# Kernel tuning notes

Measured on AMD Instinct MI355X. Metric: run time of the kernel, lower is better.

## Reference

```python
import jax, jax.numpy as jnp
import numpy as np


def setup_inputs() -> dict:
    key = jax.random.key(0)
    ks = jax.random.split(key, 16)
    B, S, D = 2, 2048, 1024
    H, SH, RH = 16, 1, 3
    hd = D // H
    w = 1.0 / np.sqrt(D)
    return {
        "x": jax.random.normal(ks[0], (B, S, D), jnp.float32),
        "Wq": jax.random.normal(ks[1], (D, D), jnp.float32) * w,
        "bq": jnp.zeros((D,), jnp.float32),
        "Wk": jax.random.normal(ks[2], (D, D), jnp.float32) * w,
        "bk": jnp.zeros((D,), jnp.float32),
        "Wv": jax.random.normal(ks[3], (D, D), jnp.float32) * w,
        "bv": jnp.zeros((D,), jnp.float32),
        "Wproj": jax.random.normal(ks[4], (D, D), jnp.float32) * w,
        "bproj": jnp.zeros((D,), jnp.float32),
        "Wr": jax.random.normal(ks[5], (D, H - SH), jnp.float32) * w,
        "br": jnp.zeros((H - SH,), jnp.float32),
        "Ws": jax.random.normal(ks[6], (D, 2), jnp.float32) * w,
        "bs": jnp.zeros((2,), jnp.float32),
        "temperature": jnp.zeros((H, 1, 1), jnp.float32),
        "query_embedding": jax.random.truncated_normal(ks[7], -2.0, 2.0, (H, 1, hd), jnp.float32) * 0.02,
        "num_heads": H,
        "shared_heads": SH,
        "routed_heads": RH,
    }


def reference(x, Wq, bq, Wk, bk, Wv, bv, Wproj, bproj, Wr, br, Ws, bs,
              temperature, query_embedding, num_heads, shared_heads, routed_heads):
    B, S, D = x.shape
    H = num_heads
    hd = D // H

    def split_heads(t):  # [B,S,D] -> [B,H,S,hd]
        return t.reshape(B, S, H, hd).transpose(0, 2, 1, 3)

    q = split_heads(x @ Wq + bq)
    k = split_heads(x @ Wk + bk)
    v = split_heads(x @ Wv + bv)

    # L2-normalize q along head_dim, add learned query embedding, scale by softplus(temperature)
    q_norm = q * jax.lax.rsqrt(jnp.sum(q * q, axis=-1, keepdims=True) + 1e-12)
    q_scaled = (q_norm + query_embedding[None]) * jax.nn.softplus(temperature)[None]

    attn = jnp.einsum('bhqd,bhkd->bhqk', q_scaled, k) / jnp.sqrt(jnp.float32(hd))
    attn = jax.nn.softmax(attn, axis=-1)
    o = jnp.einsum('bhqk,bhkd->bhqd', attn, v)
    o = o.transpose(0, 2, 1, 3).reshape(B, S, D)  # [B,S,D]

    # Routed-head gating via top-k router
    gates = jax.nn.softmax(o @ Wr + br, axis=-1)          # [B,S,H-SH]
    _, idx = jax.lax.top_k(gates, routed_heads)           # [B,S,RH]
    mask = jax.nn.one_hot(idx, H - shared_heads, dtype=gates.dtype).sum(axis=2)
    routed_gates = gates * mask * jnp.float32(routed_heads)

    # Shared-head gating
    sw = jax.nn.softmax(o @ Ws + bs, axis=-1)             # [B,S,2]
    shared_gates = sw * jnp.float32(shared_heads)
    w0 = sw * 2.0
    shared_gates = w0[..., 0:1] * shared_gates
    routed_gates = w0[..., 1:2] * routed_gates
    masked_gates = jnp.concatenate([shared_gates, routed_gates], axis=-1)

    # einsum('bnh,bnd->bnd') sums over h: scales o by sum of gates
    o = masked_gates.sum(axis=-1, keepdims=True) * o
    return o @ Wproj + bproj
```

## Files before the change

### kernel.cpp

```cpp
#include <hip/hip_runtime.h>
#include <hip/hip_bf16.h>

typedef unsigned short ushort_t;
typedef unsigned int uint_t;

typedef __attribute__((ext_vector_type(8))) short bf8;
typedef __attribute__((ext_vector_type(4))) float f4;
typedef __attribute__((ext_vector_type(16))) float f16v;

__device__ __forceinline__ float bf2f(ushort_t u) {
    unsigned int x = ((unsigned int)u) << 16;
    return __uint_as_float(x);
}
__device__ __forceinline__ ushort_t f2bf(float f) {
    unsigned int x = __float_as_uint(f);
    unsigned int r = x + 0x7fffu + ((x >> 16) & 1u);
    return (ushort_t)(r >> 16);
}
__device__ __forceinline__ uint_t pack2bf(float a, float b) {
    return (uint_t)f2bf(a) | ((uint_t)f2bf(b) << 16);
}
__device__ __forceinline__ uint_t pack2bf_fast(float a, float b) {
    uint_t au = __float_as_uint(a) + 0x8000u;
    uint_t bu = __float_as_uint(b) + 0x8000u;
    return __builtin_amdgcn_perm(bu, au, 0x07060302);
}

__device__ __forceinline__ void gl2lds16(const ushort_t* g, ushort_t* l) {
    __builtin_amdgcn_global_load_lds(
        (const __attribute__((address_space(1))) void*)g,
        (__attribute__((address_space(3))) void*)l, 16, 0, 0);
}

__global__ __launch_bounds__(256)
void prep(const float* __restrict__ x, ushort_t* __restrict__ xb,
          const float* __restrict__ Wr, const float* __restrict__ Ws,
          ushort_t* __restrict__ Wg,
          const float* __restrict__ W0, const float* __restrict__ W1,
          const float* __restrict__ W2, const float* __restrict__ W3,
          ushort_t* __restrict__ T0, ushort_t* __restrict__ T1,
          ushort_t* __restrict__ T2, ushort_t* __restrict__ T3)
{
    __shared__ float tile[32][33];
    int bid = blockIdx.x;
    int t = threadIdx.x;
    if (bid < 4096) {
        int i = bid * 256 + t;
        float4 v = ((const float4*)x)[i];
        uint2 o;
        o.x = pack2bf(v.x, v.y);
        o.y = pack2bf(v.z, v.w);
        ((uint2*)xb)[i] = o;
    } else if (bid < 4224) {
        int idx = (bid - 4096) * 256 + t;
        int c = idx >> 10, d = idx & 1023;
        float v = 0.f;
        if (c < 15) v = Wr[(size_t)d * 15 + c];
        else if (c < 17) v = Ws[(size_t)d * 2 + (c - 15)];
        Wg[idx] = f2bf(v);
    } else {
        int idx = bid - 4224;
        int z = idx >> 10, r10 = idx & 1023;
        int k0 = (r10 & 31) * 32, n0 = (r10 >> 5) * 32;
        const float* W; ushort_t* T;
        switch (z) {
            case 0: W = W0; T = T0; break;
            case 1: W = W1; T = T1; break;
            case 2: W = W2; T = T2; break;
            default: W = W3; T = T3; break;
        }
        int r = t >> 3, c4 = (t & 7) * 4;
        float4 v = *(const float4*)&W[(size_t)(k0 + r) * 1024 + n0 + c4];
        tile[r][c4 + 0] = v.x; tile[r][c4 + 1] = v.y;
        tile[r][c4 + 2] = v.z; tile[r][c4 + 3] = v.w;
        __syncthreads();
        int n = t >> 3, kk = (t & 7) * 4;
        uint2 o;
        o.x = pack2bf(tile[kk][n], tile[kk + 1][n]);
        o.y = pack2bf(tile[kk + 2][n], tile[kk + 3][n]);
        *(uint2*)&T[(size_t)(n0 + n) * 1024 + k0 + kk] = o;
    }
}

__global__ __launch_bounds__(256)
void gemmQKV(const ushort_t* __restrict__ A, const ushort_t* __restrict__ Wt3,
             const float* __restrict__ bq, const float* __restrict__ bk,
             const float* __restrict__ bv,
             ushort_t* __restrict__ Qb, ushort_t* __restrict__ Kw,
             ushort_t* __restrict__ VTw,
             const float* __restrict__ temp, const float* __restrict__ emb)
{
    const int K = 1024;
    __shared__ ushort_t As[128 * 32];
    __shared__ ushort_t Bs[128 * 32];

    int t = threadIdx.x;
    int m0 = blockIdx.x * 128;
    int y = blockIdx.y;
    int region = y >> 3;
    int n0 = (y & 7) * 128;

    int lane = t & 63, w = t >> 6;
    int lm = lane & 15, quad = lane >> 4;
    int wm = (w >> 1) * 64, wn = (w & 1) * 64;

    f4 acc[4][4] = {};

    const ushort_t* pA = &A[(size_t)(m0 + (t >> 2)) * K + (t & 3) * 8];
    const ushort_t* pB = &Wt3[(size_t)(y * 128 + (t >> 2)) * K + (t & 3) * 8];
    ushort_t* lA = &As[t * 8];
    ushort_t* lB = &Bs[t * 8];
    const size_t rstep = (size_t)64 * K;

    for (int k0 = 0; k0 < K; k0 += 32) {
        gl2lds16(pA, lA);
        gl2lds16(pA + rstep, lA + 2048);
        gl2lds16(pB, lB);
        gl2lds16(pB + rstep, lB + 2048);
        pA += 32; pB += 32;
        __syncthreads();

        bf8 af[4], bfr[4];
        #pragma unroll
        for (int mi = 0; mi < 4; mi++)
            af[mi] = *(bf8*)&As[(wm + mi * 16 + lm) * 32 + quad * 8];
        #pragma unroll
        for (int ni = 0; ni < 4; ni++)
            bfr[ni] = *(bf8*)&Bs[(wn + ni * 16 + lm) * 32 + quad * 8];
        if (region == 2) {
            #pragma unroll
            for (int mi = 0; mi < 4; mi++)
            #pragma unroll
            for (int ni = 0; ni < 4; ni++)
                acc[mi][ni] = __builtin_amdgcn_mfma_f32_16x16x32_bf16(af[mi], bfr[ni], acc[mi][ni], 0, 0, 0);
        } else {
            #pragma unroll
            for (int ni = 0; ni < 4; ni++)
            #pragma unroll
            for (int mi = 0; mi < 4; mi++)
                acc[ni][mi] = __builtin_amdgcn_mfma_f32_16x16x32_bf16(bfr[ni], af[mi], acc[ni][mi], 0, 0, 0);
        }
        __syncthreads();
    }

    if (region == 0) {
        int head = (n0 + wn) >> 6;
        float sp = log1pf(__expf(temp[head]));
        f4 bv4[4], ev4[4];
        #pragma unroll
        for (int ni = 0; ni < 4; ni++) {
            bv4[ni] = *(const f4*)&bq[n0 + wn + ni * 16 + quad * 4];
            ev4[ni] = *(const f4*)&emb[head * 64 + ni * 16 + quad * 4];
        }
        #pragma unroll
        for (int mi = 0; mi < 4; mi++) {
            float v[4][4];
            float ss = 0.f;
            #pragma unroll
            for (int ni = 0; ni < 4; ni++)
            #pragma unroll
            for (int i = 0; i < 4; i++) {
                v[ni][i] = acc[ni][mi][i] + bv4[ni][i];
                ss += v[ni][i] * v[ni][i];
            }
            ss += __shfl_xor(ss, 16, 64);
            ss += __shfl_xor(ss, 32, 64);
            float rs = rsqrtf(ss + 1e-12f);
            int tok = m0 + wm + mi * 16 + lm;
            int b = tok >> 11, s = tok & 2047;
            size_t rowb = (((size_t)(b * 16 + head)) * 2048 + s) * 64;
            #pragma unroll
            for (int ni = 0; ni < 4; ni++) {
                uint2 o;
                o.x = pack2bf((v[ni][0] * rs + ev4[ni][0]) * sp * 0.125f,
                              (v[ni][1] * rs + ev4[ni][1]) * sp * 0.125f);
                o.y = pack2bf((v[ni][2] * rs + ev4[ni][2]) * sp * 0.125f,
                              (v[ni][3] * rs + ev4[ni][3]) * sp * 0.125f);
                *(uint2*)&Qb[rowb + ni * 16 + quad * 4] = o;
            }
        }
    } else if (region == 1) {
        int head = (n0 + wn) >> 6;
        f4 bv4[4];
        #pragma unroll
        for (int ni = 0; ni < 4; ni++)
            bv4[ni] = *(const f4*)&bk[n0 + wn + ni * 16 + quad * 4];
        #pragma unroll
        for (int mi = 0; mi < 4; mi++) {
            int tok = m0 + wm + mi * 16 + lm;
            int b = tok >> 11, s = tok & 2047;
            size_t rowb = (((size_t)(b * 16 + head)) * 2048 + s) * 64;
            #pragma unroll
            for (int ni = 0; ni < 4; ni++) {
                uint2 o;
                o.x = pack2bf(acc[ni][mi][0] + bv4[ni][0], acc[ni][mi][1] + bv4[ni][1]);
                o.y = pack2bf(acc[ni][mi][2] + bv4[ni][2], acc[ni][mi][3] + bv4[ni][3]);
                *(uint2*)&Kw[rowb + ni * 16 + quad * 4] = o;
            }
        }
    } else {
        float bvv[4];
        #pragma unroll
        for (int ni = 0; ni < 4; ni++) bvv[ni] = bv[n0 + wn + ni * 16 + lm];
        #pragma unroll
        for (int mi = 0; mi < 4; mi++) {
            int gr0 = m0 + wm + mi * 16 + quad * 4;
            int b = gr0 >> 11, s0 = gr0 & 2047;
            #pragma unroll
            for (int ni = 0; ni < 4; ni++) {
                int gc = n0 + wn + ni * 16 + lm;
                int h = gc >> 6, d = gc & 63;
                uint2 o;
                o.x = pack2bf(acc[mi][ni][0] + bvv[ni], acc[mi][ni][1] + bvv[ni]);
                o.y = pack2bf(acc[mi][ni][2] + bvv[ni], acc[mi][ni][3] + bvv[ni]);
                *(uint2*)&VTw[(((size_t)(b * 16 + h)) * 64 + d) * 2048 + s0] = o;
            }
        }
    }
}

__global__ __launch_bounds__(256)
void gemmP(const ushort_t* __restrict__ A, const ushort_t* __restrict__ Wt,
           const float* __restrict__ bias, const float* __restrict__ G,
           float* __restrict__ out, int M, int N, int K)
{
    __shared__ ushort_t As[128 * 32];
    __shared__ ushort_t Bs[128 * 32];

    int t = threadIdx.x;
    int m0 = blockIdx.x * 128, n0 = blockIdx.y * 128;
    int lane = t & 63, w = t >> 6;
    int lm = lane & 15, quad = lane >> 4;
    int wm = (w >> 1) * 64, wn = (w & 1) * 64;

    f4 acc[4][4] = {};

    const ushort_t* pA = &A[(size_t)(m0 + (t >> 2)) * K + (t & 3) * 8];
    const ushort_t* pB = &Wt[(size_t)(n0 + (t >> 2)) * K + (t & 3) * 8];
    ushort_t* lA = &As[t * 8];
    ushort_t* lB = &Bs[t * 8];
    const size_t rstep = (size_t)64 * K;

    for (int k0 = 0; k0 < K; k0 += 32) {
        gl2lds16(pA, lA);
        gl2lds16(pA + rstep, lA + 2048);
        gl2lds16(pB, lB);
        gl2lds16(pB + rstep, lB + 2048);
        pA += 32; pB += 32;
        __syncthreads();

        bf8 af[4], bfr[4];
        #pragma unroll
        for (int mi = 0; mi < 4; mi++)
            af[mi] = *(bf8*)&As[(wm + mi * 16 + lm) * 32 + quad * 8];
        #pragma unroll
        for (int ni = 0; ni < 4; ni++)
            bfr[ni] = *(bf8*)&Bs[(wn + ni * 16 + lm) * 32 + quad * 8];
        #pragma unroll
        for (int ni = 0; ni < 4; ni++)
        #pragma unroll
        for (int mi = 0; mi < 4; mi++)
            acc[ni][mi] = __builtin_amdgcn_mfma_f32_16x16x32_bf16(bfr[ni], af[mi], acc[ni][mi], 0, 0, 0);
        __syncthreads();
    }

    f4 bv4[4];
    #pragma unroll
    for (int ni = 0; ni < 4; ni++)
        bv4[ni] = *(const f4*)&bias[n0 + wn + ni * 16 + quad * 4];
    #pragma unroll
    for (int mi = 0; mi < 4; mi++) {
        int tok = m0 + wm + mi * 16 + lm;
        float g = G[tok];
        size_t rowb = (size_t)tok * N + n0 + wn;
        #pragma unroll
        for (int ni = 0; ni < 4; ni++) {
            f4 o;
            #pragma unroll
            for (int i = 0; i < 4; i++) o[i] = g * acc[ni][mi][i] + bv4[ni][i];
            *(f4*)&out[rowb + ni * 16 + quad * 4] = o;
        }
    }
}

__global__ __launch_bounds__(256)
void attn(const ushort_t* __restrict__ Q, const ushort_t* __restrict__ K,
          const ushort_t* __restrict__ VT, ushort_t* __restrict__ Opart,
          float* __restrict__ Lw)
{
    __shared__ ushort_t Ks[64 * 72];
    __shared__ ushort_t Vt[64 * 72];

    int t = threadIdx.x, lane = t & 63, w = t >> 6;
    int l31 = lane & 31;
    uint_t hi = lane >> 5;
    int bid = blockIdx.x;
    int bh = bid & 31, qt = (bid >> 5) & 15, ks = bid >> 9;
    size_t base = (size_t)bh * 2048 * 64;

    int tok = qt * 128 + w * 32 + l31;
    const ushort_t* qp = &Q[base + (size_t)tok * 64 + hi * 8];
    bf8 qa[4];
    #pragma unroll
    for (int c = 0; c < 4; c++) qa[c] = *(const bf8*)(qp + c * 16);

    float l_part = 0.f;
    f16v o_acc[2] = {};

    int sr = t >> 3, sc = (t & 7) * 8;
    const ushort_t* kg0 = &K[base + (size_t)sr * 64 + sc];
    const ushort_t* vg0 = &VT[base + (size_t)sr * 2048 + sc];

    int kend = ks * 1024 + 1024;
    for (int kb = ks * 1024; kb < kend; kb += 64) {
        __syncthreads();
        {
            uint4 k0 = *(const uint4*)(kg0 + (size_t)kb * 64);
            uint4 k1 = *(const uint4*)(kg0 + (size_t)(kb + 32) * 64);
            uint4 v0 = *(const uint4*)(vg0 + kb);
            uint4 v1 = *(const uint4*)(vg0 + 32 * 2048 + kb);
            *(uint4*)&Ks[sr * 72 + sc] = k0;
            *(uint4*)&Ks[(sr + 32) * 72 + sc] = k1;
            *(uint4*)&Vt[sr * 72 + sc] = v0;
            *(uint4*)&Vt[(sr + 32) * 72 + sc] = v1;
        }
        __syncthreads();

        bf8 pf[4];
        #pragma unroll
        for (int kt2 = 0; kt2 < 2; kt2++) {
            f16v s = {};
            #pragma unroll
            for (int c = 0; c < 4; c++) {
                bf8 kf = *(bf8*)&Ks[(kt2 * 32 + l31) * 72 + c * 16 + hi * 8];
                s = __builtin_amdgcn_mfma_f32_32x32x16_bf16(kf, qa[c], s, 0, 0, 0);
            }
            uint2 pk[4];
            #pragma unroll
            for (int g = 0; g < 4; g++) {
                float p0 = __expf(s[g * 4 + 0]);
                float p1 = __expf(s[g * 4 + 1]);
                float p2 = __expf(s[g * 4 + 2]);
                float p3 = __expf(s[g * 4 + 3]);
                l_part += (p0 + p1) + (p2 + p3);
                pk[g].x = pack2bf_fast(p0, p1);
                pk[g].y = pack2bf_fast(p2, p3);
            }
            #pragma unroll
            for (int cc = 0; cc < 2; cc++) {
                uint_t sx = hi ? pk[2 * cc].x : pk[2 * cc + 1].x;
                uint_t sy = hi ? pk[2 * cc].y : pk[2 * cc + 1].y;
                uint_t rx = (uint_t)__shfl_xor((int)sx, 32, 64);
                uint_t ry = (uint_t)__shfl_xor((int)sy, 32, 64);
                uint4 u;
                u.x = hi ? rx : pk[2 * cc].x;
                u.y = hi ? ry : pk[2 * cc].y;
                u.z = hi ? pk[2 * cc + 1].x : rx;
                u.w = hi ? pk[2 * cc + 1].y : ry;
                pf[kt2 * 2 + cc] = *(bf8*)&u;
            }
        }

        #pragma unroll
        for (int c = 0; c < 4; c++) {
            #pragma unroll
            for (int dt = 0; dt < 2; dt++) {
                bf8 vf = *(bf8*)&Vt[(dt * 32 + l31) * 72 + c * 16 + hi * 8];
                o_acc[dt] = __builtin_amdgcn_mfma_f32_32x32x16_bf16(vf, pf[c], o_acc[dt], 0, 0, 0);
            }
        }
    }

    l_part += __shfl_xor(l_part, 32, 64);
    if (hi == 0) Lw[((size_t)ks * 32 + bh) * 2048 + tok] = l_part;

    size_t pbase = (((size_t)(ks * 32 + bh)) * 2048 + tok) * 64;
    #pragma unroll
    for (int dt = 0; dt < 2; dt++)
    #pragma unroll
    for (int g = 0; g < 4; g++) {
        int d0 = dt * 32 + g * 8 + hi * 4;
        uint2 o;
        o.x = pack2bf_fast(o_acc[dt][g * 4 + 0], o_acc[dt][g * 4 + 1]);
        o.y = pack2bf_fast(o_acc[dt][g * 4 + 2], o_acc[dt][g * 4 + 3]);
        *(uint2*)&Opart[pbase + d0] = o;
    }
}

__global__ __launch_bounds__(256)
void combine(const ushort_t* __restrict__ Opart, const float* __restrict__ Lw,
             ushort_t* __restrict__ Ob)
{
    int i = blockIdx.x * 256 + threadIdx.x;
    int flat = i * 4;
    int row = flat >> 6;
    int d = flat & 63;
    int bh = row >> 11, tok = row & 2047;
    int b = bh >> 4, h = bh & 15;
    float rl = 1.f / (Lw[row] + Lw[65536 + row]);
    uint2 p0 = *(const uint2*)&Opart[flat];
    uint2 p1 = *(const uint2*)&Opart[4194304 + flat];
    float v0 = (bf2f(p0.x & 0xffff) + bf2f(p1.x & 0xffff)) * rl;
    float v1 = (bf2f(p0.x >> 16)   + bf2f(p1.x >> 16))   * rl;
    float v2 = (bf2f(p0.y & 0xffff) + bf2f(p1.y & 0xffff)) * rl;
    float v3 = (bf2f(p0.y >> 16)   + bf2f(p1.y >> 16))   * rl;
    uint2 o;
    o.x = pack2bf(v0, v1);
    o.y = pack2bf(v2, v3);
    *(uint2*)&Ob[((size_t)(b * 2048 + tok)) * 1024 + h * 64 + d] = o;
}

__global__ __launch_bounds__(256)
void router(const ushort_t* __restrict__ O, const ushort_t* __restrict__ Wg,
            const float* __restrict__ br, const float* __restrict__ bs,
            float* __restrict__ G)
{
    __shared__ float Ls[64][21];
    int t = threadIdx.x, lane = t & 63, w = t >> 6;
    int lm = lane & 15, quad = lane >> 4;
    int tok0 = blockIdx.x * 64;

    const ushort_t* ap = &O[(size_t)(tok0 + w * 16 + lm) * 1024 + quad * 8];
    const ushort_t* b0p = &Wg[(size_t)lm * 1024 + quad * 8];
    const ushort_t* b1p = &Wg[(size_t)(16 + lm) * 1024 + quad * 8];

    f4 acc0 = {}, acc1 = {};
    for (int k0 = 0; k0 < 1024; k0 += 32) {
        bf8 a = *(const bf8*)(ap + k0);
        bf8 b0 = *(const bf8*)(b0p + k0);
        bf8 b1 = *(const bf8*)(b1p + k0);
        acc0 = __builtin_amdgcn_mfma_f32_16x16x32_bf16(a, b0, acc0, 0, 0, 0);
        acc1 = __builtin_amdgcn_mfma_f32_16x16x32_bf16(a, b1, acc1, 0, 0, 0);
    }
    #pragma unroll
    for (int i = 0; i < 4; i++) {
        int tl = w * 16 + quad * 4 + i;
        Ls[tl][lm] = acc0[i];
        if (lm == 0) Ls[tl][16] = acc1[i];
    }
    __syncthreads();
    if (t < 64) {
        float v[15];
        float mx = -1e30f;
        #pragma unroll
        for (int c = 0; c < 15; c++) { v[c] = Ls[t][c] + br[c]; mx = fmaxf(mx, v[c]); }
        float sum = 0.f;
        #pragma unroll
        for (int c = 0; c < 15; c++) { v[c] = __expf(v[c] - mx); sum += v[c]; }
        float inv = 1.f / sum;
        float t3 = 0.f;
        for (int r = 0; r < 3; r++) {
            int bi = 0; float bv = -1e30f;
            #pragma unroll
            for (int c = 0; c < 15; c++) if (v[c] > bv) { bv = v[c]; bi = c; }
            t3 += bv; v[bi] = -1e30f;
        }
        t3 *= inv;
        float a0 = Ls[t][15] + bs[0], a1 = Ls[t][16] + bs[1];
        float m2 = fmaxf(a0, a1);
        float e0 = __expf(a0 - m2), e1 = __expf(a1 - m2);
        G[tok0 + t] = (2.f * e0 + 6.f * e1 * t3) / (e0 + e1);
    }
}

extern "C" void kernel_launch(void* const* d_in, const int* in_sizes, int n_in,
                              void* d_out, int out_size, void* d_ws, size_t ws_size,
                              hipStream_t stream)
{
    const float* x     = (const float*)d_in[0];
    const float* Wq    = (const float*)d_in[1];
    const float* bq    = (const float*)d_in[2];
    const float* Wk    = (const float*)d_in[3];
    const float* bk    = (const float*)d_in[4];
    const float* Wv    = (const float*)d_in[5];
    const float* bv    = (const float*)d_in[6];
    const float* Wproj = (const float*)d_in[7];
    const float* bproj = (const float*)d_in[8];
    const float* Wr    = (const float*)d_in[9];
    const float* br    = (const float*)d_in[10];
    const float* Ws    = (const float*)d_in[11];
    const float* bs    = (const float*)d_in[12];
    const float* temp  = (const float*)d_in[13];
    const float* emb   = (const float*)d_in[14];

    const int M = 4096, N = 1024, Kd = 1024;

    char* ws = (char*)d_ws;
    ushort_t* Kw    = (ushort_t*)ws;
    ushort_t* VTw   = (ushort_t*)(ws + 8388608);
    ushort_t* Qb    = (ushort_t*)(ws + 16777216);
    ushort_t* Wtp   = (ushort_t*)(ws + 25165824);
    float*    Gw    = (float*)(ws + 27262976);
    ushort_t* Wg    = (ushort_t*)(ws + 27279360);
    float*    Lw    = (float*)(ws + 27344896);
    ushort_t* Wt3   = (ushort_t*)(ws + 27869184);
    ushort_t* xb    = (ushort_t*)(ws + 34160640);
    ushort_t* Opart = (ushort_t*)(ws + 27869184);
    ushort_t* Ob    = Qb;

    prep<<<8320, 256, 0, stream>>>(x, xb, Wr, Ws, Wg, Wq, Wk, Wv, Wproj,
        Wt3, Wt3 + 1048576, Wt3 + 2097152, Wtp);

    gemmQKV<<<dim3(32, 24), 256, 0, stream>>>(xb, Wt3, bq, bk, bv,
        Qb, Kw, VTw, temp, emb);

    attn<<<1024, 256, 0, stream>>>(Qb, Kw, VTw, Opart, Lw);

    combine<<<4096, 256, 0, stream>>>(Opart, Lw, Ob);

    router<<<64, 256, 0, stream>>>(Ob, Wg, br, bs, Gw);

    gemmP<<<dim3(32, 8), 256, 0, stream>>>(Ob, Wtp, bproj, Gw, (float*)d_out, M, N, Kd);
}
```

Measured before the change: 263.7 us.

## Double-buffer LDS tiles and XOR-swizzle chunks in QKV and projection GEMMs

Both bf16 MFMA GEMMs (QKV and output projection) now keep two LDS buffers. The next K-tile's global-to-LDS load is issued before the current tile is computed, so load latency can overlap the MFMAs, and one barrier per iteration is removed. The 8-element chunk index within each 32-wide row is XOR-swizzled on both store and load to cut LDS bank conflicts. The cost is double the shared memory per block, which may lower occupancy. Correctness also depends on the async LDS writes being complete before the single remaining barrier.

New measurement: 266.3 us. About the same (+1.0%).

```diff
diff --git a/kernel.cpp b/kernel.cpp
--- a/kernel.cpp
+++ b/kernel.cpp
@@ -91,8 +91,8 @@
              const float* __restrict__ temp, const float* __restrict__ emb)
 {
     const int K = 1024;
-    __shared__ ushort_t As[128 * 32];
-    __shared__ ushort_t Bs[128 * 32];
+    __shared__ ushort_t As[2][128 * 32];
+    __shared__ ushort_t Bs[2][128 * 32];
 
     int t = threadIdx.x;
     int m0 = blockIdx.x * 128;
@@ -103,30 +103,42 @@
     int lane = t & 63, w = t >> 6;
     int lm = lane & 15, quad = lane >> 4;
     int wm = (w >> 1) * 64, wn = (w & 1) * 64;
+    int swq = (quad ^ ((lm >> 1) & 3)) * 8;
 
     f4 acc[4][4] = {};
 
-    const ushort_t* pA = &A[(size_t)(m0 + (t >> 2)) * K + (t & 3) * 8];
-    const ushort_t* pB = &Wt3[(size_t)(y * 128 + (t >> 2)) * K + (t & 3) * 8];
-    ushort_t* lA = &As[t * 8];
-    ushort_t* lB = &Bs[t * 8];
+    int srow = t >> 2;
+    int schunk = ((t & 3) ^ ((srow >> 1) & 3)) * 8;
+    const ushort_t* pA = &A[(size_t)(m0 + srow) * K + schunk];
+    const ushort_t* pB = &Wt3[(size_t)(y * 128 + srow) * K + schunk];
     const size_t rstep = (size_t)64 * K;
-
+    int lofs = t * 8;
+
+    gl2lds16(pA, &As[0][lofs]);
+    gl2lds16(pA + rstep, &As[0][lofs + 2048]);
+    gl2lds16(pB, &Bs[0][lofs]);
+    gl2lds16(pB + rstep, &Bs[0][lofs + 2048]);
+    pA += 32; pB += 32;
+    __syncthreads();
+
+    int cur = 0;
     for (int k0 = 0; k0 < K; k0 += 32) {
-        gl2lds16(pA, lA);
-        gl2lds16(pA + rstep, lA + 2048);
-        gl2lds16(pB, lB);
-        gl2lds16(pB + rstep, lB + 2048);
-        pA += 32; pB += 32;
-        __syncthreads();
+        if (k0 + 32 < K) {
+            int nxt = cur ^ 1;
+            gl2lds16(pA, &As[nxt][lofs]);
+            gl2lds16(pA + rstep, &As[nxt][lofs + 2048]);
+            gl2lds16(pB, &Bs[nxt][lofs]);
+            gl2lds16(pB + rstep, &Bs[nxt][lofs + 2048]);
+            pA += 32; pB += 32;
+        }
 
         bf8 af[4], bfr[4];
         #pragma unroll
         for (int mi = 0; mi < 4; mi++)
-            af[mi] = *(bf8*)&As[(wm + mi * 16 + lm) * 32 + quad * 8];
+            af[mi] = *(bf8*)&As[cur][(wm + mi * 16 + lm) * 32 + swq];
         #pragma unroll
         for (int ni = 0; ni < 4; ni++)
-            bfr[ni] = *(bf8*)&Bs[(wn + ni * 16 + lm) * 32 + quad * 8];
+            bfr[ni] = *(bf8*)&Bs[cur][(wn + ni * 16 + lm) * 32 + swq];
         if (region == 2) {
             #pragma unroll
             for (int mi = 0; mi < 4; mi++)
@@ -141,6 +153,7 @@
                 acc[ni][mi] = __builtin_amdgcn_mfma_f32_16x16x32_bf16(bfr[ni], af[mi], acc[ni][mi], 0, 0, 0);
         }
         __syncthreads();
+        cur ^= 1;
     }
 
     if (region == 0) {
@@ -224,44 +237,57 @@
            const float* __restrict__ bias, const float* __restrict__ G,
            float* __restrict__ out, int M, int N, int K)
 {
-    __shared__ ushort_t As[128 * 32];
-    __shared__ ushort_t Bs[128 * 32];
+    __shared__ ushort_t As[2][128 * 32];
+    __shared__ ushort_t Bs[2][128 * 32];
 
     int t = threadIdx.x;
     int m0 = blockIdx.x * 128, n0 = blockIdx.y * 128;
     int lane = t & 63, w = t >> 6;
     int lm = lane & 15, quad = lane >> 4;
     int wm = (w >> 1) * 64, wn = (w & 1) * 64;
+    int swq = (quad ^ ((lm >> 1) & 3)) * 8;
 
     f4 acc[4][4] = {};
 
-    const ushort_t* pA = &A[(size_t)(m0 + (t >> 2)) * K + (t & 3) * 8];
-    const ushort_t* pB = &Wt[(size_t)(n0 + (t >> 2)) * K + (t & 3) * 8];
-    ushort_t* lA = &As[t * 8];
-    ushort_t* lB = &Bs[t * 8];
+    int srow = t >> 2;
+    int schunk = ((t & 3) ^ ((srow >> 1) & 3)) * 8;
+    const ushort_t* pA = &A[(size_t)(m0 + srow) * K + schunk];
+    const ushort_t* pB = &Wt[(size_t)(n0 + srow) * K + schunk];
     const size_t rstep = (size_t)64 * K;
-
+    int lofs = t * 8;
+
+    gl2lds16(pA, &As[0][lofs]);
+    gl2lds16(pA + rstep, &As[0][lofs + 2048]);
+    gl2lds16(pB, &Bs[0][lofs]);
+    gl2lds16(pB + rstep, &Bs[0][lofs + 2048]);
+    pA += 32; pB += 32;
+    __syncthreads();
+
+    int cur = 0;
     for (int k0 = 0; k0 < K; k0 += 32) {
-        gl2lds16(pA, lA);
-        gl2lds16(pA + rstep, lA + 2048);
-        gl2lds16(pB, lB);
-        gl2lds16(pB + rstep, lB + 2048);
-        pA += 32; pB += 32;
-        __syncthreads();
+        if (k0 + 32 < K) {
+            int nxt = cur ^ 1;
+            gl2lds16(pA, &As[nxt][lofs]);
+            gl2lds16(pA + rstep, &As[nxt][lofs + 2048]);
+            gl2lds16(pB, &Bs[nxt][lofs]);
+            gl2lds16(pB + rstep, &Bs[nxt][lofs + 2048]);
+            pA += 32; pB += 32;
+        }
 
         bf8 af[4], bfr[4];
         #pragma unroll
         for (int mi = 0; mi < 4; mi++)
-            af[mi] = *(bf8*)&As[(wm + mi * 16 + lm) * 32 + quad * 8];
+            af[mi] = *(bf8*)&As[cur][(wm + mi * 16 + lm) * 32 + swq];
         #pragma unroll
         for (int ni = 0; ni < 4; ni++)
-            bfr[ni] = *(bf8*)&Bs[(wn + ni * 16 + lm) * 32 + quad * 8];
+            bfr[ni] = *(bf8*)&Bs[cur][(wn + ni * 16 + lm) * 32 + swq];
         #pragma unroll
         for (int ni = 0; ni < 4; ni++)
         #pragma unroll
         for (int mi = 0; mi < 4; mi++)
             acc[ni][mi] = __builtin_amdgcn_mfma_f32_16x16x32_bf16(bfr[ni], af[mi], acc[ni][mi], 0, 0, 0);
         __syncthreads();
+        cur ^= 1;
     }
 
     f4 bv4[4];
```
